# Kernel optimization log

Hardware: AMD Instinct MI355X
Metric: run time of the kernel (lower is better)

The kernel has to match this reference:

```python
import jax, jax.numpy as jnp
import numpy as np

N_QUBITS = 10
N_LAYERS = 3
OUT_MIN, OUT_MAX = -0.1, 0.1


def _apply_1q(state, U, wire):
    # state: (B, 2**n) complex64; U: (2,2) complex64 gate on `wire` (wire 0 = MSB, PennyLane order)
    B = state.shape[0]
    s = state.reshape(B, 2 ** wire, 2, -1)
    s = jnp.einsum('ij,bljr->blir', U, s)
    return s.reshape(B, -1)


def _apply_ry_batched(state, theta, wire):
    # per-sample RY(theta) on `wire`; theta: (B,)
    B = state.shape[0]
    s = state.reshape(B, 2 ** wire, 2, -1)
    c = jnp.cos(0.5 * theta)[:, None, None]
    si = jnp.sin(0.5 * theta)[:, None, None]
    a0, a1 = s[:, :, 0, :], s[:, :, 1, :]
    s = jnp.stack([c * a0 - si * a1, si * a0 + c * a1], axis=2)
    return s.reshape(B, -1)


def _apply_cnot(state, ctrl):
    # CNOT with control=ctrl, target=ctrl+1 (adjacent wires)
    B = state.shape[0]
    s = state.reshape(B, 2 ** ctrl, 2, 2, -1)
    s = jnp.stack([s[:, :, 0], s[:, :, 1, ::-1]], axis=2)
    return s.reshape(B, -1)


def _circuit(z, weights):
    # Faithful statevector simulation of the PennyLane qnode, batched over samples.
    B = z.shape[0]
    n = N_QUBITS
    state = jnp.zeros((B, 2 ** n), jnp.complex64).at[:, 0].set(1.0)
    zc = jnp.clip(z, -1.0, 1.0)
    for i in range(n):
        state = _apply_ry_batched(state, zc[:, i % zc.shape[1]], i)
    # Fuse RZ(a)->RY(b)->RZ(c) per (layer, qubit) into one 2x2 unitary: U = Rz(c) @ Ry(b) @ Rz(a)
    a, b, c = weights[..., 0], weights[..., 1], weights[..., 2]
    ea, eap = jnp.exp(-0.5j * a), jnp.exp(0.5j * a)
    ec, ecp = jnp.exp(-0.5j * c), jnp.exp(0.5j * c)
    cb, sb = jnp.cos(0.5 * b), jnp.sin(0.5 * b)
    U = jnp.stack([jnp.stack([ec * cb * ea, -ec * sb * eap], -1),
                   jnp.stack([ecp * sb * ea, ecp * cb * eap], -1)], -2)  # (L, Q, 2, 2)
    U = U.astype(jnp.complex64)
    for l in range(N_LAYERS):
        for i in range(n):
            state = _apply_1q(state, U[l, i], i)
        for i in range(n - 1):
            state = _apply_cnot(state, i)
    probs = jnp.abs(state) ** 2  # (B, 2**n) float32
    feats = []
    for i in range(n):
        p = probs.reshape(B, 2 ** i, 2, -1)
        feats.append(p[:, :, 0].sum((1, 2)) - p[:, :, 1].sum((1, 2)))  # <Z_i>
    return jnp.stack(feats, -1)  # (B, n_qubits)


def setup_inputs() -> dict:
    key = jax.random.key(0)
    ks = jax.random.split(key, 8)
    B = 4096
    return {
        'z': jax.random.normal(ks[0], (B, N_QUBITS), jnp.float32),
        'weights': jax.random.normal(ks[1], (N_LAYERS, N_QUBITS, 3), jnp.float32) * 0.01,
        'W1': jax.random.normal(ks[2], (N_QUBITS, 32), jnp.float32) * 0.3,
        'b1': jax.random.normal(ks[3], (32,), jnp.float32) * 0.05,
        'W2': jax.random.normal(ks[4], (32, 16), jnp.float32) * 0.2,
        'b2': jax.random.normal(ks[5], (16,), jnp.float32) * 0.05,
        'W3': jax.random.normal(ks[6], (16, 1), jnp.float32) * 0.2,
        'b3': jax.random.normal(ks[7], (1,), jnp.float32) * 0.05,
    }


def reference(z, weights, W1, b1, W2, b2, W3, b3):
    feats = _circuit(z, weights)                  # (B, n_qubits)
    h = jnp.tanh(feats @ W1 + b1)
    h = jnp.tanh(h @ W2 + b2)
    raw = h @ W3 + b3                             # (B, 1)
    return jax.nn.sigmoid(raw) * (OUT_MAX - OUT_MIN) + OUT_MIN
```

## Files before the change

### kernel.cpp

```cpp
#include <hip/hip_runtime.h>

namespace {

constexpr int NQ = 10;

struct cplx { float re, im; };

__device__ __forceinline__ cplx cmul(cplx a, cplx b) {
  return cplx{ fmaf(a.re, b.re, -a.im * b.im), fmaf(a.re, b.im, a.im * b.re) };
}
__device__ __forceinline__ cplx cmadd2(cplx u, cplx a, cplx v, cplx b) {
  cplx r;
  r.re = fmaf(u.re, a.re, fmaf(-u.im, a.im, fmaf(v.re, b.re, -v.im * b.im)));
  r.im = fmaf(u.re, a.im, fmaf( u.im, a.re, fmaf(v.re, b.im,  v.im * b.re)));
  return r;
}
__device__ __forceinline__ cplx csel(bool c, cplx x, cplx y) {
  return cplx{ c ? x.re : y.re, c ? x.im : y.im };
}

__device__ __forceinline__ float fast_tanh(float x) {
  float xc = fminf(fmaxf(x, -10.f), 10.f);
  float e = __expf(2.f * xc);
  return __fdividef(e - 1.f, e + 1.f);
}

__device__ __forceinline__ float rdlane(float v, int l) {
  return __int_as_float(__builtin_amdgcn_readlane(__float_as_int(v), l));
}
template<int CTRL>
__device__ __forceinline__ float dppf(float v) {
  return __int_as_float(__builtin_amdgcn_update_dpp(0, __float_as_int(v), CTRL, 0xF, 0xF, true));
}
template<int CTRL>
__device__ __forceinline__ cplx dppc(cplx v) { return cplx{ dppf<CTRL>(v.re), dppf<CTRL>(v.im) }; }
template<int C1, int C2>
__device__ __forceinline__ cplx dppc2(cplx v) { return dppc<C2>(dppc<C1>(v)); }

template<int PAT>
__device__ __forceinline__ float swzf(float v) {
  return __int_as_float(__builtin_amdgcn_ds_swizzle(__float_as_int(v), PAT));
}
template<int PAT>
__device__ __forceinline__ cplx swzc(cplx v) { return cplx{ swzf<PAT>(v.re), swzf<PAT>(v.im) }; }
__device__ __forceinline__ cplx shflxc(cplx v, int m) {
  return cplx{ __shfl_xor(v.re, m), __shfl_xor(v.im, m) };
}

struct Umat { float r00,i00,r01,i01,r10,i10,r11,i11; };
__device__ __forceinline__ void getU(const Umat& m, int g,
                                     cplx& u00, cplx& u01, cplx& u10, cplx& u11) {
  u00 = cplx{rdlane(m.r00, g), rdlane(m.i00, g)};
  u01 = cplx{rdlane(m.r01, g), rdlane(m.i01, g)};
  u10 = cplx{rdlane(m.r10, g), rdlane(m.i10, g)};
  u11 = cplx{rdlane(m.r11, g), rdlane(m.i11, g)};
}

template<int LX, int HIL>
__device__ __forceinline__ void gate_shfl(cplx (&amp)[16], int lane, cplx u00,cplx u01,cplx u10,cplx u11) {
  bool hi = (__popc(lane & HIL) & 1) != 0;
  cplx cA = csel(hi, u11, u00), cB = csel(hi, u10, u01);
  #pragma unroll
  for (int t = 0; t < 16; ++t) amp[t] = cmadd2(cA, amp[t], cB, shflxc(amp[t], LX));
}
template<int PAT, int HIL>
__device__ __forceinline__ void gate_swz(cplx (&amp)[16], int lane, cplx u00,cplx u01,cplx u10,cplx u11) {
  bool hi = (__popc(lane & HIL) & 1) != 0;
  cplx cA = csel(hi, u11, u00), cB = csel(hi, u10, u01);
  #pragma unroll
  for (int t = 0; t < 16; ++t) amp[t] = cmadd2(cA, amp[t], cB, swzc<PAT>(amp[t]));
}
template<int C1, int HIL>
__device__ __forceinline__ void gate_dpp1(cplx (&amp)[16], int lane, cplx u00,cplx u01,cplx u10,cplx u11) {
  bool hi = (__popc(lane & HIL) & 1) != 0;
  cplx cA = csel(hi, u11, u00), cB = csel(hi, u10, u01);
  #pragma unroll
  for (int t = 0; t < 16; ++t) amp[t] = cmadd2(cA, amp[t], cB, dppc<C1>(amp[t]));
}
template<int C1, int C2, int HIL>
__device__ __forceinline__ void gate_dpp2(cplx (&amp)[16], int lane, cplx u00,cplx u01,cplx u10,cplx u11) {
  bool hi = (__popc(lane & HIL) & 1) != 0;
  cplx cA = csel(hi, u11, u00), cB = csel(hi, u10, u01);
  #pragma unroll
  for (int t = 0; t < 16; ++t) amp[t] = cmadd2(cA, amp[t], cB, dppc2<C1,C2>(amp[t]));
}
template<int CTRL, int LOCX, int HIL>
__device__ __forceinline__ void gate_mixed(cplx (&amp)[16], int lane, cplx u00,cplx u01,cplx u10,cplx u11) {
  bool hi = (__popc(lane & HIL) & 1) != 0;
  cplx cA = csel(hi, u11, u00), cB = csel(hi, u10, u01);
  #pragma unroll
  for (int t0 = 0; t0 < 16; ++t0) {
    if (t0 & LOCX) continue;
    const int t1 = t0 | LOCX;
    cplx o0 = dppc<CTRL>(amp[t1]);
    cplx o1 = dppc<CTRL>(amp[t0]);
    amp[t0] = cmadd2(cA, amp[t0], cB, o0);
    amp[t1] = cmadd2(cA, amp[t1], cB, o1);
  }
}
constexpr int hbit(int m) { return m >= 8 ? 8 : (m >= 4 ? 4 : (m >= 2 ? 2 : 1)); }
template<int PLOC, int HIL, int HILOC>
__device__ __forceinline__ void gate_local(cplx (&amp)[16], int lane, cplx u00,cplx u01,cplx u10,cplx u11) {
  bool h0 = (__popc(lane & HIL) & 1) != 0;
  cplx cA0 = csel(h0, u11, u00), cB0 = csel(h0, u10, u01);
  cplx cA1 = csel(h0, u00, u11), cB1 = csel(h0, u01, u10);
  #pragma unroll
  for (int ta = 0; ta < 16; ++ta) {
    if (ta & hbit(PLOC)) continue;
    const int tb = ta ^ PLOC;
    const bool pa = (__popc(ta & HILOC) & 1) != 0;
    cplx aA = amp[ta], aB = amp[tb];
    if (!pa) { amp[ta] = cmadd2(cA0, aA, cB0, aB); amp[tb] = cmadd2(cA1, aB, cB1, aA); }
    else     { amp[ta] = cmadd2(cA1, aA, cB1, aB); amp[tb] = cmadd2(cA0, aB, cB0, aA); }
  }
}

__device__ __forceinline__ float wht6(float v, float s1, float s2, float s4,
                                      float s8, float s16, float s32) {
  float o;
  o = dppf<0xB1>(v);               v = fmaf(s1,  v, o);
  o = dppf<0x4E>(v);               v = fmaf(s2,  v, o);
  o = dppf<0x1B>(dppf<0x141>(v));  v = fmaf(s4,  v, o);
  o = dppf<0x128>(v);              v = fmaf(s8,  v, o);
  o = swzf<0x401F>(v);             v = fmaf(s16, v, o);
  o = __shfl_xor(v, 32);           v = fmaf(s32, v, o);
  return v;
}

__global__ __launch_bounds__(256, 4)
void qgan_kernel(const float* __restrict__ z, const float* __restrict__ wts,
                 const float* __restrict__ W1, const float* __restrict__ b1,
                 const float* __restrict__ W2, const float* __restrict__ b2,
                 const float* __restrict__ W3, const float* __restrict__ b3,
                 float* __restrict__ out, int B)
{
  const int tid  = blockIdx.x * 256 + threadIdx.x;
  const int lane = threadIdx.x & 63;
  const int wv   = __builtin_amdgcn_readfirstlane(tid >> 6);
  if (wv >= B) return;

  const int j32 = lane & 31, k16 = lane & 15;
  float w1r[10];
  #pragma unroll
  for (int i = 0; i < NQ; ++i) w1r[i] = W1[i * 32 + j32];
  float b1v = b1[j32], b2v = b2[k16], w3v = W3[k16], b3v = b3[0];

  Umat m;
  {
    int g = (lane < 30) ? lane : 0;
    float wa = wts[g * 3 + 0], wb = wts[g * 3 + 1], wc = wts[g * 3 + 2];
    float al = 0.5f * (wa + wc), be = 0.5f * (wa - wc), hb = 0.5f * wb;
    float ca = __cosf(al),  sa = __sinf(al);
    float cbe = __cosf(be), sbe = __sinf(be);
    float cb = __cosf(hb),  sb = __sinf(hb);
    m.r00 =  cb * ca;  m.i00 = -cb * sa;
    m.r01 = -sb * cbe; m.i01 = -sb * sbe;
    m.r10 =  sb * cbe; m.i10 = -sb * sbe;
    m.r11 =  cb * ca;  m.i11 =  cb * sa;
  }

  cplx u00, u01, u10, u11;
  const float* zp = z + wv * NQ;

  cplx laneF = {1.f, 0.f};
  #pragma unroll
  for (int q = 0; q < 6; ++q) {
    float zz = fminf(fmaxf(zp[q], -1.f), 1.f);
    float c0 = __cosf(0.5f * zz), s0 = __sinf(0.5f * zz);
    getU(m, q, u00, u01, u10, u11);
    cplx va = { fmaf(u00.re, c0, u01.re * s0), fmaf(u00.im, c0, u01.im * s0) };
    cplx vb = { fmaf(u10.re, c0, u11.re * s0), fmaf(u10.im, c0, u11.im * s0) };
    cplx f = csel((lane >> (5 - q)) & 1, vb, va);
    laneF = (q == 0) ? f : cmul(laneF, f);
  }
  cplx va_[4], vb_[4];
  #pragma unroll
  for (int q = 6; q < 10; ++q) {
    float zz = fminf(fmaxf(zp[q], -1.f), 1.f);
    float c0 = __cosf(0.5f * zz), s0 = __sinf(0.5f * zz);
    getU(m, q, u00, u01, u10, u11);
    va_[q - 6] = { fmaf(u00.re, c0, u01.re * s0), fmaf(u00.im, c0, u01.im * s0) };
    vb_[q - 6] = { fmaf(u10.re, c0, u11.re * s0), fmaf(u10.im, c0, u11.im * s0) };
  }

  cplx amp[16];
  {
    cplx P2[4];
    P2[0] = cmul(va_[2], va_[3]);
    P2[1] = cmul(va_[2], vb_[3]);
    P2[2] = cmul(vb_[2], va_[3]);
    P2[3] = cmul(vb_[2], vb_[3]);
    cplx g0 = cmul(laneF, va_[0]);
    cplx g1 = cmul(laneF, vb_[0]);
    #pragma unroll
    for (int t = 0; t < 16; ++t) {
      cplx t7 = ((t >> 2) & 1) ? vb_[1] : va_[1];
      cplx tt = cmul(t7, P2[t & 3]);
      amp[t] = cmul(((t >> 3) & 1) ? g1 : g0, tt);
    }
  }

  getU(m, 10, u00,u01,u10,u11); gate_shfl <0x30, 0x20>(amp, lane, u00,u01,u10,u11);
  getU(m, 11, u00,u01,u10,u11); gate_swz  <0x601F, 0x30>(amp, lane, u00,u01,u10,u11);
  getU(m, 12, u00,u01,u10,u11); gate_dpp2 <0x140, 0x1B, 0x38>(amp, lane, u00,u01,u10,u11);
  getU(m, 13, u00,u01,u10,u11); gate_dpp2 <0x141, 0xB1, 0x3C>(amp, lane, u00,u01,u10,u11);
  getU(m, 14, u00,u01,u10,u11); gate_dpp1 <0x1B, 0x3E>(amp, lane, u00,u01,u10,u11);
  getU(m, 15, u00,u01,u10,u11); gate_mixed<0xB1, 8, 0x3F>(amp, lane, u00,u01,u10,u11);
  getU(m, 16, u00,u01,u10,u11); gate_local<0xC, 0x3F, 0x8>(amp, lane, u00,u01,u10,u11);
  getU(m, 17, u00,u01,u10,u11); gate_local<0x6, 0x3F, 0xC>(amp, lane, u00,u01,u10,u11);
  getU(m, 18, u00,u01,u10,u11); gate_local<0x3, 0x3F, 0xE>(amp, lane, u00,u01,u10,u11);
  getU(m, 19, u00,u01,u10,u11); gate_local<0x1, 0x3F, 0xF>(amp, lane, u00,u01,u10,u11);

  getU(m, 20, u00,u01,u10,u11); gate_shfl <0x28, 0x20>(amp, lane, u00,u01,u10,u11);
  getU(m, 21, u00,u01,u10,u11); gate_swz  <0x501F, 0x10>(amp, lane, u00,u01,u10,u11);
  getU(m, 22, u00,u01,u10,u11); gate_dpp2 <0x128, 0x4E, 0x28>(amp, lane, u00,u01,u10,u11);
  getU(m, 23, u00,u01,u10,u11); gate_dpp2 <0x141, 0x4E, 0x14>(amp, lane, u00,u01,u10,u11);
  getU(m, 24, u00,u01,u10,u11); gate_mixed<0x4E, 8, 0x2A>(amp, lane, u00,u01,u10,u11);
  getU(m, 25, u00,u01,u10,u11); gate_mixed<0xB1, 4, 0x15>(amp, lane, u00,u01,u10,u11);
  getU(m, 26, u00,u01,u10,u11); gate_local<0xA, 0x2A, 0x8>(amp, lane, u00,u01,u10,u11);
  getU(m, 27, u00,u01,u10,u11); gate_local<0x5, 0x15, 0x4>(amp, lane, u00,u01,u10,u11);
  getU(m, 28, u00,u01,u10,u11); gate_local<0x2, 0x2A, 0xA>(amp, lane, u00,u01,u10,u11);
  getU(m, 29, u00,u01,u10,u11); gate_local<0x1, 0x15, 0x5>(amp, lane, u00,u01,u10,u11);

  float w2r[32];
  #pragma unroll
  for (int jj = 0; jj < 32; ++jj) w2r[jj] = W2[jj * 16 + k16];

  float p[16];
  #pragma unroll
  for (int t = 0; t < 16; ++t)
    p[t] = fmaf(amp[t].re, amp[t].re, amp[t].im * amp[t].im);

  #pragma unroll
  for (int k = 1; k <= 8; k <<= 1) {
    #pragma unroll
    for (int t = 0; t < 16; ++t) {
      if (t & k) continue;
      float a = p[t], b = p[t | k];
      p[t] = a + b; p[t | k] = a - b;
    }
  }

  float s1  = (lane & 1)  ? -1.f : 1.f;
  float s2  = (lane & 2)  ? -1.f : 1.f;
  float s4  = (lane & 4)  ? -1.f : 1.f;
  float s8  = (lane & 8)  ? -1.f : 1.f;
  float s16 = (lane & 16) ? -1.f : 1.f;
  float s32 = (lane & 32) ? -1.f : 1.f;
  float B0 = wht6(p[0],   s1,s2,s4,s8,s16,s32);
  float B8 = wht6(p[8],   s1,s2,s4,s8,s16,s32);
  float BC = wht6(p[0xC], s1,s2,s4,s8,s16,s32);
  float B6 = wht6(p[6],   s1,s2,s4,s8,s16,s32);
  float B3 = wht6(p[3],   s1,s2,s4,s8,s16,s32);

  float f0 = rdlane(B0, 0x20), f1 = rdlane(B0, 0x30);
  float f2 = rdlane(B0, 0x18), f3 = rdlane(B0, 0x0C);
  float f4 = rdlane(B0, 0x26), f5 = rdlane(B0, 0x33);
  float f6 = rdlane(B8, 0x19), f7 = rdlane(BC, 0x0C);
  float f8 = rdlane(B6, 0x26), f9 = rdlane(B3, 0x33);
  float feats[10] = {f0,f1,f2,f3,f4,f5,f6,f7,f8,f9};

  float acc = b1v;
  #pragma unroll
  for (int i = 0; i < NQ; ++i) acc = fmaf(feats[i], w1r[i], acc);
  float h1 = fast_tanh(acc);

  float acc2 = b2v;
  #pragma unroll
  for (int jj = 0; jj < 32; ++jj)
    acc2 = fmaf(rdlane(h1, jj), w2r[jj], acc2);
  float h2 = fast_tanh(acc2);

  float vv = h2 * w3v;
  vv += dppf<0xB1>(vv);
  vv += dppf<0x4E>(vv);
  vv += dppf<0x1B>(dppf<0x141>(vv));
  vv += dppf<0x128>(vv);

  if (lane == 0) out[wv] = 0.1f * fast_tanh(0.5f * (vv + b3v));
}

}

extern "C" void kernel_launch(void* const* d_in, const int* in_sizes, int n_in,
                              void* d_out, int out_size, void* d_ws, size_t ws_size,
                              hipStream_t stream) {
  const float* z   = (const float*)d_in[0];
  const float* wts = (const float*)d_in[1];
  const float* W1  = (const float*)d_in[2];
  const float* b1  = (const float*)d_in[3];
  const float* W2  = (const float*)d_in[4];
  const float* b2  = (const float*)d_in[5];
  const float* W3  = (const float*)d_in[6];
  const float* b3  = (const float*)d_in[7];
  float* out = (float*)d_out;
  (void)d_ws; (void)ws_size;

  int B = in_sizes[0] / NQ;
  int blocks = (B + 3) / 4;
  hipLaunchKernelGGL(qgan_kernel, dim3(blocks), dim3(256), 0, stream,
                     z, wts, W1, b1, W2, b2, W3, b3, out, B);
}
```

Before: 95.46 us.

## Replace specialized cross-lane gates with runtime bpermute loop; one-wave blocks

```diff
diff --git a/kernel.cpp b/kernel.cpp
--- a/kernel.cpp
+++ b/kernel.cpp
@@ -34,17 +34,13 @@
 }
 template<int CTRL>
 __device__ __forceinline__ cplx dppc(cplx v) { return cplx{ dppf<CTRL>(v.re), dppf<CTRL>(v.im) }; }
-template<int C1, int C2>
-__device__ __forceinline__ cplx dppc2(cplx v) { return dppc<C2>(dppc<C1>(v)); }
 
 template<int PAT>
 __device__ __forceinline__ float swzf(float v) {
   return __int_as_float(__builtin_amdgcn_ds_swizzle(__float_as_int(v), PAT));
 }
-template<int PAT>
-__device__ __forceinline__ cplx swzc(cplx v) { return cplx{ swzf<PAT>(v.re), swzf<PAT>(v.im) }; }
-__device__ __forceinline__ cplx shflxc(cplx v, int m) {
-  return cplx{ __shfl_xor(v.re, m), __shfl_xor(v.im, m) };
+__device__ __forceinline__ float bperm(int addr, float v) {
+  return __int_as_float(__builtin_amdgcn_ds_bpermute(addr, __float_as_int(v)));
 }
 
 struct Umat { float r00,i00,r01,i01,r10,i10,r11,i11; };
@@ -56,34 +52,19 @@
   u11 = cplx{rdlane(m.r11, g), rdlane(m.i11, g)};
 }
 
-template<int LX, int HIL>
-__device__ __forceinline__ void gate_shfl(cplx (&amp)[16], int lane, cplx u00,cplx u01,cplx u10,cplx u11) {
+__device__ __forceinline__ void gate_lane_rt(cplx (&amp)[16], int lane, const Umat& m,
+                                             int g, int LX, int HIL) {
+  cplx u00, u01, u10, u11; getU(m, g, u00, u01, u10, u11);
   bool hi = (__popc(lane & HIL) & 1) != 0;
   cplx cA = csel(hi, u11, u00), cB = csel(hi, u10, u01);
-  #pragma unroll
-  for (int t = 0; t < 16; ++t) amp[t] = cmadd2(cA, amp[t], cB, shflxc(amp[t], LX));
-}
-template<int PAT, int HIL>
-__device__ __forceinline__ void gate_swz(cplx (&amp)[16], int lane, cplx u00,cplx u01,cplx u10,cplx u11) {
-  bool hi = (__popc(lane & HIL) & 1) != 0;
-  cplx cA = csel(hi, u11, u00), cB = csel(hi, u10, u01);
-  #pragma unroll
-  for (int t = 0; t < 16; ++t) amp[t] = cmadd2(cA, amp[t], cB, swzc<PAT>(amp[t]));
-}
-template<int C1, int HIL>
-__device__ __forceinline__ void gate_dpp1(cplx (&amp)[16], int lane, cplx u00,cplx u01,cplx u10,cplx u11) {
-  bool hi = (__popc(lane & HIL) & 1) != 0;
-  cplx cA = csel(hi, u11, u00), cB = csel(hi, u10, u01);
-  #pragma unroll
-  for (int t = 0; t < 16; ++t) amp[t] = cmadd2(cA, amp[t], cB, dppc<C1>(amp[t]));
-}
-template<int C1, int C2, int HIL>
-__device__ __forceinline__ void gate_dpp2(cplx (&amp)[16], int lane, cplx u00,cplx u01,cplx u10,cplx u11) {
-  bool hi = (__popc(lane & HIL) & 1) != 0;
-  cplx cA = csel(hi, u11, u00), cB = csel(hi, u10, u01);
-  #pragma unroll
-  for (int t = 0; t < 16; ++t) amp[t] = cmadd2(cA, amp[t], cB, dppc2<C1,C2>(amp[t]));
-}
+  const int addr = (lane ^ LX) << 2;
+  float ore[16], oim[16];
+  #pragma unroll
+  for (int t = 0; t < 16; ++t) { ore[t] = bperm(addr, amp[t].re); oim[t] = bperm(addr, amp[t].im); }
+  #pragma unroll
+  for (int t = 0; t < 16; ++t) amp[t] = cmadd2(cA, amp[t], cB, cplx{ore[t], oim[t]});
+}
+
 template<int CTRL, int LOCX, int HIL>
 __device__ __forceinline__ void gate_mixed(cplx (&amp)[16], int lane, cplx u00,cplx u01,cplx u10,cplx u11) {
   bool hi = (__popc(lane & HIL) & 1) != 0;
@@ -127,16 +108,23 @@
   return v;
 }
 
-__global__ __launch_bounds__(256, 4)
+constexpr int pk6(int a, int b, int c, int d, int e) {
+  return a | (b << 6) | (c << 12) | (d << 18) | (e << 24);
+}
+constexpr int LX1  = pk6(0x30, 0x18, 0x0C, 0x06, 0x03);
+constexpr int HIL1 = pk6(0x20, 0x30, 0x38, 0x3C, 0x3E);
+constexpr int LX2  = pk6(0x28, 0x14, 0x0A, 0x05, 0);
+constexpr int HIL2 = pk6(0x20, 0x10, 0x28, 0x14, 0);
+
+__global__ __launch_bounds__(64, 4)
 void qgan_kernel(const float* __restrict__ z, const float* __restrict__ wts,
                  const float* __restrict__ W1, const float* __restrict__ b1,
                  const float* __restrict__ W2, const float* __restrict__ b2,
                  const float* __restrict__ W3, const float* __restrict__ b3,
                  float* __restrict__ out, int B)
 {
-  const int tid  = blockIdx.x * 256 + threadIdx.x;
-  const int lane = threadIdx.x & 63;
-  const int wv   = __builtin_amdgcn_readfirstlane(tid >> 6);
+  const int lane = threadIdx.x;
+  const int wv   = blockIdx.x;
   if (wv >= B) return;
 
   const int j32 = lane & 31, k16 = lane & 15;
@@ -200,21 +188,18 @@
     }
   }
 
-  getU(m, 10, u00,u01,u10,u11); gate_shfl <0x30, 0x20>(amp, lane, u00,u01,u10,u11);
-  getU(m, 11, u00,u01,u10,u11); gate_swz  <0x601F, 0x30>(amp, lane, u00,u01,u10,u11);
-  getU(m, 12, u00,u01,u10,u11); gate_dpp2 <0x140, 0x1B, 0x38>(amp, lane, u00,u01,u10,u11);
-  getU(m, 13, u00,u01,u10,u11); gate_dpp2 <0x141, 0xB1, 0x3C>(amp, lane, u00,u01,u10,u11);
-  getU(m, 14, u00,u01,u10,u11); gate_dpp1 <0x1B, 0x3E>(amp, lane, u00,u01,u10,u11);
+  #pragma unroll 1
+  for (int i = 0; i < 5; ++i)
+    gate_lane_rt(amp, lane, m, 10 + i, (LX1 >> (6 * i)) & 63, (HIL1 >> (6 * i)) & 63);
   getU(m, 15, u00,u01,u10,u11); gate_mixed<0xB1, 8, 0x3F>(amp, lane, u00,u01,u10,u11);
   getU(m, 16, u00,u01,u10,u11); gate_local<0xC, 0x3F, 0x8>(amp, lane, u00,u01,u10,u11);
   getU(m, 17, u00,u01,u10,u11); gate_local<0x6, 0x3F, 0xC>(amp, lane, u00,u01,u10,u11);
   getU(m, 18, u00,u01,u10,u11); gate_local<0x3, 0x3F, 0xE>(amp, lane, u00,u01,u10,u11);
   getU(m, 19, u00,u01,u10,u11); gate_local<0x1, 0x3F, 0xF>(amp, lane, u00,u01,u10,u11);
 
-  getU(m, 20, u00,u01,u10,u11); gate_shfl <0x28, 0x20>(amp, lane, u00,u01,u10,u11);
-  getU(m, 21, u00,u01,u10,u11); gate_swz  <0x501F, 0x10>(amp, lane, u00,u01,u10,u11);
-  getU(m, 22, u00,u01,u10,u11); gate_dpp2 <0x128, 0x4E, 0x28>(amp, lane, u00,u01,u10,u11);
-  getU(m, 23, u00,u01,u10,u11); gate_dpp2 <0x141, 0x4E, 0x14>(amp, lane, u00,u01,u10,u11);
+  #pragma unroll 1
+  for (int i = 0; i < 4; ++i)
+    gate_lane_rt(amp, lane, m, 20 + i, (LX2 >> (6 * i)) & 63, (HIL2 >> (6 * i)) & 63);
   getU(m, 24, u00,u01,u10,u11); gate_mixed<0x4E, 8, 0x2A>(amp, lane, u00,u01,u10,u11);
   getU(m, 25, u00,u01,u10,u11); gate_mixed<0xB1, 4, 0x15>(amp, lane, u00,u01,u10,u11);
   getU(m, 26, u00,u01,u10,u11); gate_local<0xA, 0x2A, 0x8>(amp, lane, u00,u01,u10,u11);
@@ -253,12 +238,12 @@
   float B6 = wht6(p[6],   s1,s2,s4,s8,s16,s32);
   float B3 = wht6(p[3],   s1,s2,s4,s8,s16,s32);
 
-  float f0 = rdlane(B0, 0x20), f1 = rdlane(B0, 0x30);
-  float f2 = rdlane(B0, 0x18), f3 = rdlane(B0, 0x0C);
-  float f4 = rdlane(B0, 0x26), f5 = rdlane(B0, 0x33);
-  float f6 = rdlane(B8, 0x19), f7 = rdlane(BC, 0x0C);
-  float f8 = rdlane(B6, 0x26), f9 = rdlane(B3, 0x33);
-  float feats[10] = {f0,f1,f2,f3,f4,f5,f6,f7,f8,f9};
+  float feats[10];
+  feats[0] = rdlane(B0, 0x20); feats[1] = rdlane(B0, 0x30);
+  feats[2] = rdlane(B0, 0x18); feats[3] = rdlane(B0, 0x0C);
+  feats[4] = rdlane(B0, 0x26); feats[5] = rdlane(B0, 0x33);
+  feats[6] = rdlane(B8, 0x19); feats[7] = rdlane(BC, 0x0C);
+  feats[8] = rdlane(B6, 0x26); feats[9] = rdlane(B3, 0x33);
 
   float acc = b1v;
   #pragma unroll
@@ -297,7 +282,6 @@
   (void)d_ws; (void)ws_size;
 
   int B = in_sizes[0] / NQ;
-  int blocks = (B + 3) / 4;
-  hipLaunchKernelGGL(qgan_kernel, dim3(blocks), dim3(256), 0, stream,
+  hipLaunchKernelGGL(qgan_kernel, dim3(B), dim3(64), 0, stream,
                      z, wts, W1, b1, W2, b2, W3, b3, out, B);
 }
```

After: 92.58 us. 3.0% less time.
